# Kernel optimization log

Hardware: AMD Instinct MI355X
Metric: run time of the kernel (lower is better)

## Reference

```python
import jax, jax.numpy as jnp
import numpy as np

N = 8192
C_IN = 512
C_INTER = 128  # in_channels // unit_nums = 512 // 4


def setup_inputs() -> dict:
    key = jax.random.key(0)
    ks = jax.random.split(key, 6)
    x = jax.random.normal(ks[0], (N, C_IN), dtype=jnp.float32)
    # Linear weights init: normal(0, 0.01); biases zero. Stored as [in, out].
    Wg = 0.01 * jax.random.normal(ks[1], (C_IN, C_INTER), dtype=jnp.float32)
    Wt = 0.01 * jax.random.normal(ks[2], (C_IN, C_INTER), dtype=jnp.float32)
    Wp = 0.01 * jax.random.normal(ks[3], (C_IN, C_INTER), dtype=jnp.float32)
    bg = jnp.zeros((C_INTER,), dtype=jnp.float32)
    bt = jnp.zeros((C_INTER,), dtype=jnp.float32)
    bp = jnp.zeros((C_INTER,), dtype=jnp.float32)
    # 1x1 conv weight (1, 2*C_INTER, 1, 1) flattened: first half hits theta, second half phi
    wcat = 0.01 * jax.random.normal(ks[4], (2 * C_INTER,), dtype=jnp.float32)
    return {"x": x, "Wg": Wg, "bg": bg, "Wt": Wt, "bt": bt, "Wp": Wp, "bp": bp, "wcat": wcat}


def reference(x, Wg, bg, Wt, bt, Wp, bp, wcat):
    n = x.shape[0]
    g_x = x @ Wg + bg          # [N, C_inter]
    theta = x @ Wt + bt        # [N, C_inter]
    phi = x @ Wp + bp          # [N, C_inter]
    c = theta.shape[1]
    # 1x1 conv over cat([theta_i, phi_j]) == w1.theta_i + w2.phi_j (outer sum), then ReLU
    a = theta @ wcat[:c]       # [N]
    b = phi @ wcat[c:]         # [N]
    f = jax.nn.relu(a[:, None] + b[None, :])  # [N, N]
    z = (f / n) @ g_x          # [N, C_inter]
    return z
```

## Files before the change

kernel.cpp:

```cpp
#include <hip/hip_runtime.h>

#define C_IN   512
#define C_INT  128
#define NBUCK  8192
#define SEG    32
#define NSEG   256

typedef short short8 __attribute__((ext_vector_type(8)));
typedef float floatx4 __attribute__((ext_vector_type(4)));


__device__ __forceinline__ int bucket_of(float v, float bmin, float inv_w) {
    float fk = (v - bmin) * inv_w;
    fk = fminf(fmaxf(fk, 0.f), (float)(NBUCK - 1));
    return (int)fk;
}

__device__ __forceinline__ short bf16rnd(float v) {
    unsigned u = __float_as_uint(v);
    return (short)((u + 0x7fffu + ((u >> 16) & 1u)) >> 16);
}


__global__ __launch_bounds__(256) void prep_kernel(
        const float* __restrict__ Wt, const float* __restrict__ Wp,
        const float* __restrict__ Wg, const float* __restrict__ wcat,
        const float* __restrict__ bt, const float* __restrict__ bp,
        float* __restrict__ ut, float* __restrict__ up, float* __restrict__ scal,
        unsigned short* __restrict__ WgT) {
    int t = threadIdx.x, bk = blockIdx.x;
    if (bk < 16) {
        const float* W  = (bk < 8) ? Wt : Wp;
        const float* wv = wcat + ((bk < 8) ? 0 : C_INT);
        float* dst      = (bk < 8) ? ut : up;
        int k = (bk & 7) * 64 + (t >> 2);
        int q = t & 3;
        const float4* row = (const float4*)(W + (size_t)k * C_INT);
        const float4* cv4 = (const float4*)wv;
        float s = 0.f;
        #pragma unroll
        for (int i = 0; i < 8; ++i) {
            float4 a = row[q * 8 + i];
            float4 c = cv4[q * 8 + i];
            s += a.x * c.x + a.y * c.y + a.z * c.z + a.w * c.w;
        }
        s += __shfl_xor(s, 1);
        s += __shfl_xor(s, 2);
        if (q == 0) dst[k] = s;
    } else if (bk == 16) {
        float s1p = (t < C_INT) ? bt[t] * wcat[t] : 0.f;
        float s2p = (t < C_INT) ? bp[t] * wcat[C_INT + t] : 0.f;
        for (int off = 32; off; off >>= 1) {
            s1p += __shfl_down(s1p, off);
            s2p += __shfl_down(s2p, off);
        }
        __shared__ float red[8];
        int w = t >> 6, lane = t & 63;
        if (lane == 0) { red[w] = s1p; red[4 + w] = s2p; }
        __syncthreads();
        if (t == 0) {
            scal[0] = red[0] + red[1] + red[2] + red[3];
            scal[1] = red[4] + red[5] + red[6] + red[7];
        }
    } else {
        __shared__ float tile[64][132];
        int kb = (bk - 17) * 64;
        #pragma unroll
        for (int it = 0; it < 8; ++it) {
            int idx = it * 256 + t;
            int r = idx >> 5, c4 = idx & 31;
            *(float4*)&tile[r][c4 * 4] =
                ((const float4*)(Wg + (size_t)(kb + r) * C_INT))[c4];
        }
        __syncthreads();
        int n = t & 127, kc = (t >> 7) * 32;
        unsigned pk[16];
        #pragma unroll
        for (int i = 0; i < 16; ++i) {
            unsigned lo = (unsigned short)bf16rnd(tile[kc + 2 * i][n]);
            unsigned hi = (unsigned short)bf16rnd(tile[kc + 2 * i + 1][n]);
            pk[i] = lo | (hi << 16);
        }
        uint4* dst = (uint4*)(WgT + (size_t)n * C_IN + kb + kc);
        #pragma unroll
        for (int i2 = 0; i2 < 4; ++i2) dst[i2] = *(uint4*)&pk[i2 * 4];
    }
}


#define RSTR 66

__global__ __launch_bounds__(256) void gemm_mfma(
        const float* __restrict__ x, const unsigned short* __restrict__ WgT,
        const float* __restrict__ bg,
        const float* __restrict__ ut, const float* __restrict__ up,
        const float* __restrict__ scal,
        _Float16* __restrict__ g, float* __restrict__ a, float* __restrict__ b) {
    __shared__ float red[3][12][RSTR];
    int tid = threadIdx.x;
    int lane = tid & 63, wv = tid >> 6;
    int bx = blockIdx.x;
    int cg2 = bx >> 9;
    int i0 = (bx & 511) * 16;
    int m = lane & 15, q = lane >> 4;
    floatx4 accg[2] = {};
    floatx4 accab = {};
    const float* xrow = x + (size_t)(i0 + m) * C_IN + q * 8;
    const float* absrc = (m == 0) ? ut : up;
    #pragma unroll
    for (int ks = 0; ks < 4; ++ks) {
        int k0 = (wv * 4 + ks) * 32;
        float4 f0 = *(const float4*)(xrow + k0);
        float4 f1 = *(const float4*)(xrow + k0 + 4);
        short8 af;
        af[0] = bf16rnd(f0.x); af[1] = bf16rnd(f0.y);
        af[2] = bf16rnd(f0.z); af[3] = bf16rnd(f0.w);
        af[4] = bf16rnd(f1.x); af[5] = bf16rnd(f1.y);
        af[6] = bf16rnd(f1.z); af[7] = bf16rnd(f1.w);
        if (cg2 == 0) {
            short8 abf = {};
            if (m < 2) {
                float4 u0 = *(const float4*)(absrc + k0 + q * 8);
                float4 u1 = *(const float4*)(absrc + k0 + q * 8 + 4);
                abf[0] = bf16rnd(u0.x); abf[1] = bf16rnd(u0.y);
                abf[2] = bf16rnd(u0.z); abf[3] = bf16rnd(u0.w);
                abf[4] = bf16rnd(u1.x); abf[5] = bf16rnd(u1.y);
                abf[6] = bf16rnd(u1.z); abf[7] = bf16rnd(u1.w);
            }
            accab = __builtin_amdgcn_mfma_f32_16x16x32_bf16(af, abf, accab, 0, 0, 0);
        }
        #pragma unroll
        for (int f = 0; f < 2; ++f) {
            short8 bfr = *(const short8*)(WgT + (size_t)(cg2 * 32 + f * 16 + m) * C_IN + k0 + q * 8);
            accg[f] = __builtin_amdgcn_mfma_f32_16x16x32_bf16(af, bfr, accg[f], 0, 0, 0);
        }
    }
    if (wv) {
        #pragma unroll
        for (int f = 0; f < 2; ++f)
            #pragma unroll
            for (int r = 0; r < 4; ++r)
                red[wv - 1][f * 4 + r][lane] = accg[f][r];
        #pragma unroll
        for (int r = 0; r < 4; ++r)
            red[wv - 1][8 + r][lane] = accab[r];
    }
    __syncthreads();
    if (wv == 0) {
        #pragma unroll
        for (int w = 0; w < 3; ++w) {
            #pragma unroll
            for (int f = 0; f < 2; ++f)
                #pragma unroll
                for (int r = 0; r < 4; ++r)
                    accg[f][r] += red[w][f * 4 + r][lane];
            #pragma unroll
            for (int r = 0; r < 4; ++r)
                accab[r] += red[w][8 + r][lane];
        }
        #pragma unroll
        for (int f = 0; f < 2; ++f) {
            int col = cg2 * 32 + f * 16 + m;
            float bgv = bg[col];
            #pragma unroll
            for (int r = 0; r < 4; ++r) {
                int row = i0 + q * 4 + r;
                g[(size_t)row * C_INT + col] = (_Float16)(accg[f][r] + bgv);
            }
        }
        if (cg2 == 0 && m < 2) {
            float off = m ? scal[1] : scal[0];
            float* dst = m ? b : a;
            #pragma unroll
            for (int r = 0; r < 4; ++r) dst[i0 + q * 4 + r] = accab[r] + off;
        }
    }
}


__global__ __launch_bounds__(1024) void sort_kernel(
        const float* __restrict__ b, float* __restrict__ scal,
        unsigned* __restrict__ offs_g, unsigned short* __restrict__ perm_g,
        float* __restrict__ bsort_g) {
    __shared__ unsigned oh[NBUCK / 2];
    __shared__ unsigned cur[NBUCK / 2];
    __shared__ unsigned short ls[8192];
    __shared__ unsigned wtu[16];
    __shared__ float smn[16], smx[16], sbp[2];
    int t = threadIdx.x, lane = t & 63, wv = t >> 6;
    #pragma unroll
    for (int r = 0; r < 4; ++r) { oh[t + r * 1024] = 0u; cur[t + r * 1024] = 0u; }
    float bv[8];
    float mn = 1e30f, mx = -1e30f;
    #pragma unroll
    for (int r = 0; r < 8; ++r) {
        bv[r] = b[t + r * 1024];
        mn = fminf(mn, bv[r]); mx = fmaxf(mx, bv[r]);
    }
    for (int off = 32; off; off >>= 1) {
        mn = fminf(mn, __shfl_down(mn, off));
        mx = fmaxf(mx, __shfl_down(mx, off));
    }
    if (lane == 0) { smn[wv] = mn; smx[wv] = mx; }
    __syncthreads();
    if (t == 0) {
        float gmn = smn[0], gmx = smx[0];
        #pragma unroll
        for (int i = 1; i < 16; ++i) {
            gmn = fminf(gmn, smn[i]); gmx = fmaxf(gmx, smx[i]);
        }
        float range = gmx - gmn;
        float iw = (range > 1e-30f) ? (float)NBUCK / range : 0.f;
        sbp[0] = gmn; sbp[1] = iw;
        scal[4] = gmn; scal[5] = iw;
    }
    __syncthreads();
    float bmin = sbp[0], inv_w = sbp[1];
    int kb[8];
    #pragma unroll
    for (int r = 0; r < 8; ++r) {
        kb[r] = bucket_of(bv[r], bmin, inv_w);
        atomicAdd(&oh[kb[r] >> 1], (kb[r] & 1) ? 0x10000u : 1u);
    }
    __syncthreads();
    unsigned h[8], p = 0;
    #pragma unroll
    for (int w = 0; w < 4; ++w) {
        unsigned word = oh[t * 4 + w];
        p += word & 0xffffu;  h[w * 2]     = p;
        p += word >> 16;      h[w * 2 + 1] = p;
    }
    unsigned v = p;
    #pragma unroll
    for (int d = 1; d < 64; d <<= 1) {
        unsigned u = __shfl_up(v, d);
        if (lane >= d) v += u;
    }
    if (lane == 63) wtu[wv] = v;
    __syncthreads();
    if (t < 16) {
        unsigned w = wtu[t];
        #pragma unroll
        for (int d = 1; d < 16; d <<= 1) {
            unsigned u = __shfl_up(w, d);
            if (t >= d) w += u;
        }
        wtu[t] = w;
    }
    __syncthreads();
    unsigned base = (v - p) + (wv ? wtu[wv - 1] : 0u);
    #pragma unroll
    for (int w = 0; w < 4; ++w) {
        unsigned lo = base + h[w * 2], hi = base + h[w * 2 + 1];
        oh[t * 4 + w] = lo | (hi << 16);
        offs_g[t * 8 + w * 2 + 1] = lo;
        offs_g[t * 8 + w * 2 + 2] = hi;
    }
    if (t == 0) offs_g[0] = 0u;
    __syncthreads();
    #pragma unroll
    for (int r = 0; r < 8; ++r) {
        int j = t + r * 1024;
        int k = kb[r];
        unsigned st = 0u;
        if (k > 0) {
            unsigned word = oh[(k - 1) >> 1];
            st = ((k - 1) & 1) ? (word >> 16) : (word & 0xffffu);
        }
        unsigned old = atomicAdd(&cur[k >> 1], (k & 1) ? 0x10000u : 1u);
        unsigned pos = (k & 1) ? (old >> 16) : (old & 0xffffu);
        ls[st + pos] = (unsigned short)j;
    }
    __syncthreads();
    #pragma unroll
    for (int r = 0; r < 8; ++r) {
        int e = t + r * 1024;
        int j = ls[e];
        perm_g[e] = (unsigned short)j;
        bsort_g[e] = b[j];
    }
}


__global__ __launch_bounds__(128) void segsum_kernel(
        const _Float16* __restrict__ g, const unsigned short* __restrict__ perm,
        const float* __restrict__ bsort,
        float* __restrict__ seg1, float* __restrict__ seg2) {
    __shared__ int pj[SEG];
    __shared__ float pb[SEG];
    int s = blockIdx.x, t = threadIdx.x;
    if (t < SEG) { pj[t] = perm[s * SEG + t]; pb[t] = bsort[s * SEG + t]; }
    __syncthreads();
    float a1 = 0.f, a2 = 0.f;
    #pragma unroll
    for (int e = 0; e < SEG; ++e) {
        float gv = (float)g[(size_t)pj[e] * C_INT + t];
        a1 += gv; a2 += pb[e] * gv;
    }
    seg1[s * C_INT + t] = a1;
    seg2[s * C_INT + t] = a2;
}


__global__ __launch_bounds__(1024) void sufseg_kernel(
        const float* __restrict__ seg1, const float* __restrict__ seg2,
        float* __restrict__ Suf1, float* __restrict__ Suf2) {
    __shared__ float ps1[8][128], ps2[8][128];
    int t = threadIdx.x, u = t >> 7, c = t & 127;
    float p1 = 0.f, p2 = 0.f;
    #pragma unroll 8
    for (int j = 0; j < 32; ++j) {
        int s = u * 32 + j;
        p1 += seg1[s * C_INT + c];
        p2 += seg2[s * C_INT + c];
    }
    ps1[u][c] = p1; ps2[u][c] = p2;
    __syncthreads();
    float r1 = 0.f, r2 = 0.f;
    #pragma unroll
    for (int u2 = u + 1; u2 < 8; ++u2) { r1 += ps1[u2][c]; r2 += ps2[u2][c]; }
    for (int j = 31; j >= 0; --j) {
        int s = u * 32 + j;
        r1 += seg1[s * C_INT + c];
        r2 += seg2[s * C_INT + c];
        Suf1[s * C_INT + c] = r1;
        Suf2[s * C_INT + c] = r2;
    }
    if (t < 128) {
        Suf1[256 * C_INT + t] = 0.f; Suf2[256 * C_INT + t] = 0.f;
        Suf1[257 * C_INT + t] = 0.f; Suf2[257 * C_INT + t] = 0.f;
    }
}


__global__ __launch_bounds__(128) void out_kernel(
        const float* __restrict__ a, const float* __restrict__ scal,
        const _Float16* __restrict__ g,
        const unsigned* __restrict__ offs, const unsigned short* __restrict__ perm,
        const float* __restrict__ bsort,
        const float* __restrict__ Suf1, const float* __restrict__ Suf2,
        float* __restrict__ out, float inv_n) {
    int i = blockIdx.x, c = threadIdx.x;
    float ai = a[i], thr = -ai;
    float bmin = scal[4], inv_w = scal[5];
    int ki = bucket_of(thr, bmin, inv_w);
    unsigned e0 = offs[ki], e1 = offs[ki + 1];
    unsigned s1 = e1 >> 5;
    unsigned segend = min((s1 + 1u) * 32u, (unsigned)NBUCK);
    size_t sb = (size_t)(s1 + 1u) * C_INT + c;
    float acc = ai * Suf1[sb] + Suf2[sb];
    for (unsigned e = e1; e < segend; ++e) {
        float bj = bsort[e];
        int j = perm[e];
        acc += (ai + bj) * (float)g[(size_t)j * C_INT + c];
    }
    for (unsigned e = e0; e < e1; ++e) {
        float bj = bsort[e];
        if (bj > thr) {
            int j = perm[e];
            acc += (ai + bj) * (float)g[(size_t)j * C_INT + c];
        }
    }
    out[(size_t)i * C_INT + c] = acc * inv_n;
}


extern "C" void kernel_launch(void* const* d_in, const int* in_sizes, int n_in,
                              void* d_out, int out_size, void* d_ws, size_t ws_size,
                              hipStream_t stream) {
    const float* x    = (const float*)d_in[0];
    const float* Wg   = (const float*)d_in[1];
    const float* bg   = (const float*)d_in[2];
    const float* Wt   = (const float*)d_in[3];
    const float* bt   = (const float*)d_in[4];
    const float* Wp   = (const float*)d_in[5];
    const float* bp   = (const float*)d_in[6];
    const float* wcat = (const float*)d_in[7];
    float* out = (float*)d_out;
    int n = in_sizes[0] / C_IN;

    char* w = (char*)d_ws;
    size_t off = 0;
    auto alloc = [&](size_t bytes) -> void* {
        void* p = w + off;
        off += (bytes + 255) & ~(size_t)255;
        return p;
    };
    float*          ut    = (float*)alloc(C_IN * 4);
    float*          up    = (float*)alloc(C_IN * 4);
    float*          scal  = (float*)alloc(32);
    float*          a     = (float*)alloc((size_t)n * 4);
    float*          b     = (float*)alloc((size_t)n * 4);
    unsigned*       offs  = (unsigned*)alloc((size_t)(NBUCK + 1) * 4);
    unsigned short* perm  = (unsigned short*)alloc((size_t)n * 2);
    float*          bsort = (float*)alloc((size_t)n * 4);
    _Float16*       g     = (_Float16*)alloc((size_t)n * C_INT * 2);
    unsigned short* WgT   = (unsigned short*)alloc((size_t)C_INT * C_IN * 2);
    float*          seg1  = (float*)alloc((size_t)NSEG * C_INT * 4);
    float*          seg2  = (float*)alloc((size_t)NSEG * C_INT * 4);
    float*          Suf1  = (float*)alloc((size_t)258 * C_INT * 4);
    float*          Suf2  = (float*)alloc((size_t)258 * C_INT * 4);

    prep_kernel<<<25, 256, 0, stream>>>(Wt, Wp, Wg, wcat, bt, bp, ut, up, scal, WgT);
    gemm_mfma<<<2048, 256, 0, stream>>>(x, WgT, bg, ut, up, scal, g, a, b);
    sort_kernel<<<1, 1024, 0, stream>>>(b, scal, offs, perm, bsort);
    segsum_kernel<<<NSEG, 128, 0, stream>>>(g, perm, bsort, seg1, seg2);
    sufseg_kernel<<<1, 1024, 0, stream>>>(seg1, seg2, Suf1, Suf2);
    out_kernel<<<n, 128, 0, stream>>>(a, scal, g, offs, perm, bsort, Suf1, Suf2,
                                      out, 1.0f / (float)n);
}
```

Before: 140.4 us.

## Fuse segment-sum and suffix-scan kernels with last-block atomic completion

Merges segsum and sufseg into one kernel. The new kernel uses 32 blocks of 1024 threads, each covering 8 segments, and the last block to finish (found via an atomic counter) computes the suffix sums. This removes one kernel launch and its inter-kernel gap. The cost is fewer, larger blocks for the gather-sum phase, an extra counter reset added to prep_kernel, and reliance on threadfence ordering for correctness.

```diff
diff --git a/kernel.cpp b/kernel.cpp
--- a/kernel.cpp
+++ b/kernel.cpp
@@ -27,7 +27,7 @@
         const float* __restrict__ Wg, const float* __restrict__ wcat,
         const float* __restrict__ bt, const float* __restrict__ bp,
         float* __restrict__ ut, float* __restrict__ up, float* __restrict__ scal,
-        unsigned short* __restrict__ WgT) {
+        unsigned short* __restrict__ WgT, unsigned* __restrict__ cnt) {
     int t = threadIdx.x, bk = blockIdx.x;
     if (bk < 16) {
         const float* W  = (bk < 8) ? Wt : Wp;
@@ -62,7 +62,7 @@
             scal[0] = red[0] + red[1] + red[2] + red[3];
             scal[1] = red[4] + red[5] + red[6] + red[7];
         }
-    } else {
+    } else if (bk < 25) {
         __shared__ float tile[64][132];
         int kb = (bk - 17) * 64;
         #pragma unroll
@@ -84,6 +84,8 @@
         uint4* dst = (uint4*)(WgT + (size_t)n * C_IN + kb + kc);
         #pragma unroll
         for (int i2 = 0; i2 < 4; ++i2) dst[i2] = *(uint4*)&pk[i2 * 4];
+    } else {
+        if (t == 0) *cnt = 0u;
     }
 }
 
@@ -282,37 +284,46 @@
 }
 
 
-__global__ __launch_bounds__(128) void segsum_kernel(
+__global__ __launch_bounds__(1024) void segsum_kernel(
         const _Float16* __restrict__ g, const unsigned short* __restrict__ perm,
         const float* __restrict__ bsort,
-        float* __restrict__ seg1, float* __restrict__ seg2) {
-    __shared__ int pj[SEG];
-    __shared__ float pb[SEG];
-    int s = blockIdx.x, t = threadIdx.x;
-    if (t < SEG) { pj[t] = perm[s * SEG + t]; pb[t] = bsort[s * SEG + t]; }
-    __syncthreads();
+        float* __restrict__ seg1, float* __restrict__ seg2,
+        float* __restrict__ Suf1, float* __restrict__ Suf2,
+        unsigned* __restrict__ cnt) {
+    __shared__ int pj[8][SEG];
+    __shared__ float pb[8][SEG];
+    __shared__ float ps1[8][128], ps2[8][128];
+    __shared__ unsigned lastFlag;
+    int blk = blockIdx.x, t = threadIdx.x;
+    int u = t >> 7, c = t & 127;
+    if (t < 256) {
+        pj[t >> 5][t & 31] = perm[blk * 256 + t];
+        pb[t >> 5][t & 31] = bsort[blk * 256 + t];
+    }
+    __syncthreads();
+    int s = blk * 8 + u;
     float a1 = 0.f, a2 = 0.f;
     #pragma unroll
     for (int e = 0; e < SEG; ++e) {
-        float gv = (float)g[(size_t)pj[e] * C_INT + t];
-        a1 += gv; a2 += pb[e] * gv;
-    }
-    seg1[s * C_INT + t] = a1;
-    seg2[s * C_INT + t] = a2;
-}
-
-
-__global__ __launch_bounds__(1024) void sufseg_kernel(
-        const float* __restrict__ seg1, const float* __restrict__ seg2,
-        float* __restrict__ Suf1, float* __restrict__ Suf2) {
-    __shared__ float ps1[8][128], ps2[8][128];
-    int t = threadIdx.x, u = t >> 7, c = t & 127;
+        float gv = (float)g[(size_t)pj[u][e] * C_INT + c];
+        a1 += gv; a2 += pb[u][e] * gv;
+    }
+    seg1[s * C_INT + c] = a1;
+    seg2[s * C_INT + c] = a2;
+    __threadfence();
+    __syncthreads();
+    if (t == 0)
+        lastFlag = (__hip_atomic_fetch_add(cnt, 1u, __ATOMIC_ACQ_REL,
+                                           __HIP_MEMORY_SCOPE_AGENT) == 31u);
+    __syncthreads();
+    if (!lastFlag) return;
+    __threadfence();
     float p1 = 0.f, p2 = 0.f;
     #pragma unroll 8
     for (int j = 0; j < 32; ++j) {
-        int s = u * 32 + j;
-        p1 += seg1[s * C_INT + c];
-        p2 += seg2[s * C_INT + c];
+        int s2 = u * 32 + j;
+        p1 += seg1[s2 * C_INT + c];
+        p2 += seg2[s2 * C_INT + c];
     }
     ps1[u][c] = p1; ps2[u][c] = p2;
     __syncthreads();
@@ -320,11 +331,11 @@
     #pragma unroll
     for (int u2 = u + 1; u2 < 8; ++u2) { r1 += ps1[u2][c]; r2 += ps2[u2][c]; }
     for (int j = 31; j >= 0; --j) {
-        int s = u * 32 + j;
-        r1 += seg1[s * C_INT + c];
-        r2 += seg2[s * C_INT + c];
-        Suf1[s * C_INT + c] = r1;
-        Suf2[s * C_INT + c] = r2;
+        int s2 = u * 32 + j;
+        r1 += seg1[s2 * C_INT + c];
+        r2 += seg2[s2 * C_INT + c];
+        Suf1[s2 * C_INT + c] = r1;
+        Suf2[s2 * C_INT + c] = r2;
     }
     if (t < 128) {
         Suf1[256 * C_INT + t] = 0.f; Suf2[256 * C_INT + t] = 0.f;
@@ -400,12 +411,14 @@
     float*          seg2  = (float*)alloc((size_t)NSEG * C_INT * 4);
     float*          Suf1  = (float*)alloc((size_t)258 * C_INT * 4);
     float*          Suf2  = (float*)alloc((size_t)258 * C_INT * 4);
-
-    prep_kernel<<<25, 256, 0, stream>>>(Wt, Wp, Wg, wcat, bt, bp, ut, up, scal, WgT);
+    unsigned*       cnt   = (unsigned*)alloc(256);
+
+    prep_kernel<<<26, 256, 0, stream>>>(Wt, Wp, Wg, wcat, bt, bp, ut, up, scal,
+                                        WgT, cnt);
     gemm_mfma<<<2048, 256, 0, stream>>>(x, WgT, bg, ut, up, scal, g, a, b);
     sort_kernel<<<1, 1024, 0, stream>>>(b, scal, offs, perm, bsort);
-    segsum_kernel<<<NSEG, 128, 0, stream>>>(g, perm, bsort, seg1, seg2);
-    sufseg_kernel<<<1, 1024, 0, stream>>>(seg1, seg2, Suf1, Suf2);
+    segsum_kernel<<<32, 1024, 0, stream>>>(g, perm, bsort, seg1, seg2,
+                                           Suf1, Suf2, cnt);
     out_kernel<<<n, 128, 0, stream>>>(a, scal, g, offs, perm, bsort, Suf1, Suf2,
                                       out, 1.0f / (float)n);
 }
```

Result: slower. 156.4 us (+11.4%).

## Fuse sort into the GEMM launch and compute a/b projections in prep

Applied to the files above, without the earlier changes.

The projections a and b are now computed in fp32 inside the prep kernel. Each of its 128 blocks recomputes the folded theta/phi weight vectors, then takes dot products with its rows of x. The single-block bucket sort now runs as block 0 of a combined launch whose other blocks do the g GEMM, so the sort can overlap the GEMM instead of running alone as a serial kernel. In exchange, x is read twice, the folded weights are recomputed redundantly per block, and the GEMM now uses 1024-thread blocks that share one LDS union with the sort.

```diff
diff --git a/kernel.cpp b/kernel.cpp
--- a/kernel.cpp
+++ b/kernel.cpp
@@ -26,45 +26,57 @@
         const float* __restrict__ Wt, const float* __restrict__ Wp,
         const float* __restrict__ Wg, const float* __restrict__ wcat,
         const float* __restrict__ bt, const float* __restrict__ bp,
-        float* __restrict__ ut, float* __restrict__ up, float* __restrict__ scal,
+        const float* __restrict__ x,
+        float* __restrict__ a, float* __restrict__ b,
         unsigned short* __restrict__ WgT) {
     int t = threadIdx.x, bk = blockIdx.x;
-    if (bk < 16) {
-        const float* W  = (bk < 8) ? Wt : Wp;
-        const float* wv = wcat + ((bk < 8) ? 0 : C_INT);
-        float* dst      = (bk < 8) ? ut : up;
-        int k = (bk & 7) * 64 + (t >> 2);
-        int q = t & 3;
-        const float4* row = (const float4*)(W + (size_t)k * C_INT);
-        const float4* cv4 = (const float4*)wv;
-        float s = 0.f;
-        #pragma unroll
-        for (int i = 0; i < 8; ++i) {
-            float4 a = row[q * 8 + i];
-            float4 c = cv4[q * 8 + i];
-            s += a.x * c.x + a.y * c.y + a.z * c.z + a.w * c.w;
-        }
-        s += __shfl_xor(s, 1);
-        s += __shfl_xor(s, 2);
-        if (q == 0) dst[k] = s;
-    } else if (bk == 16) {
-        float s1p = (t < C_INT) ? bt[t] * wcat[t] : 0.f;
-        float s2p = (t < C_INT) ? bp[t] * wcat[C_INT + t] : 0.f;
-        for (int off = 32; off; off >>= 1) {
-            s1p += __shfl_down(s1p, off);
-            s2p += __shfl_down(s2p, off);
-        }
-        __shared__ float red[8];
-        int w = t >> 6, lane = t & 63;
-        if (lane == 0) { red[w] = s1p; red[4 + w] = s2p; }
-        __syncthreads();
-        if (t == 0) {
-            scal[0] = red[0] + red[1] + red[2] + red[3];
-            scal[1] = red[4] + red[5] + red[6] + red[7];
-        }
+    if (bk < 128) {
+        __shared__ float utl[512], upl[512];
+        __shared__ float sred[2];
+        #pragma unroll
+        for (int h = 0; h < 2; ++h) {
+            int k = t + h * 256;
+            const float4* wr = (const float4*)(Wt + (size_t)k * C_INT);
+            const float4* pr = (const float4*)(Wp + (size_t)k * C_INT);
+            const float4* c1 = (const float4*)wcat;
+            const float4* c2 = (const float4*)(wcat + C_INT);
+            float s1 = 0.f, s2 = 0.f;
+            #pragma unroll
+            for (int j = 0; j < 32; ++j) {
+                float4 w4 = wr[j], q4 = pr[j], a4 = c1[j], b4 = c2[j];
+                s1 += w4.x * a4.x + w4.y * a4.y + w4.z * a4.z + w4.w * a4.w;
+                s2 += q4.x * b4.x + q4.y * b4.y + q4.z * b4.z + q4.w * b4.w;
+            }
+            utl[k] = s1; upl[k] = s2;
+        }
+        {
+            float v = 0.f;
+            if (t < 64)        v = bt[t] * wcat[t] + bt[t + 64] * wcat[t + 64];
+            else if (t < 128) { int c = t - 64;
+                               v = bp[c] * wcat[C_INT + c] + bp[c + 64] * wcat[C_INT + c + 64]; }
+            for (int off = 32; off; off >>= 1) v += __shfl_down(v, off);
+            if (t < 128 && (t & 63) == 0) sred[t >> 6] = v;
+        }
+        __syncthreads();
+        float s0 = sred[0], s1c = sred[1];
+        int r = t >> 2, kq = t & 3;
+        int i = bk * 64 + r;
+        const float4* xr = (const float4*)(x + (size_t)i * C_IN + kq * 128);
+        const float4* u4 = (const float4*)(utl + kq * 128);
+        const float4* p4 = (const float4*)(upl + kq * 128);
+        float sa = 0.f, sb = 0.f;
+        #pragma unroll
+        for (int j = 0; j < 32; ++j) {
+            float4 xv = xr[j], uv = u4[j], pv = p4[j];
+            sa += xv.x * uv.x + xv.y * uv.y + xv.z * uv.z + xv.w * uv.w;
+            sb += xv.x * pv.x + xv.y * pv.y + xv.z * pv.z + xv.w * pv.w;
+        }
+        sa += __shfl_xor(sa, 1); sa += __shfl_xor(sa, 2);
+        sb += __shfl_xor(sb, 1); sb += __shfl_xor(sb, 2);
+        if (kq == 0) { a[i] = sa + s0; b[i] = sb + s1c; }
     } else {
         __shared__ float tile[64][132];
-        int kb = (bk - 17) * 64;
+        int kb = (bk - 128) * 64;
         #pragma unroll
         for (int it = 0; it < 8; ++it) {
             int idx = it * 256 + t;
@@ -90,194 +102,175 @@
 
 #define RSTR 66
 
-__global__ __launch_bounds__(256) void gemm_mfma(
+struct SortLDS {
+    unsigned oh[NBUCK / 2];
+    unsigned cur[NBUCK / 2];
+    unsigned short ls[8192];
+    unsigned wtu[16];
+    float smn[16], smx[16], sbp[2];
+};
+
+__global__ __launch_bounds__(1024) void gst_kernel(
         const float* __restrict__ x, const unsigned short* __restrict__ WgT,
-        const float* __restrict__ bg,
-        const float* __restrict__ ut, const float* __restrict__ up,
-        const float* __restrict__ scal,
-        _Float16* __restrict__ g, float* __restrict__ a, float* __restrict__ b) {
-    __shared__ float red[3][12][RSTR];
-    int tid = threadIdx.x;
-    int lane = tid & 63, wv = tid >> 6;
-    int bx = blockIdx.x;
-    int cg2 = bx >> 9;
-    int i0 = (bx & 511) * 16;
-    int m = lane & 15, q = lane >> 4;
-    floatx4 accg[2] = {};
-    floatx4 accab = {};
-    const float* xrow = x + (size_t)(i0 + m) * C_IN + q * 8;
-    const float* absrc = (m == 0) ? ut : up;
-    #pragma unroll
-    for (int ks = 0; ks < 4; ++ks) {
-        int k0 = (wv * 4 + ks) * 32;
-        float4 f0 = *(const float4*)(xrow + k0);
-        float4 f1 = *(const float4*)(xrow + k0 + 4);
-        short8 af;
-        af[0] = bf16rnd(f0.x); af[1] = bf16rnd(f0.y);
-        af[2] = bf16rnd(f0.z); af[3] = bf16rnd(f0.w);
-        af[4] = bf16rnd(f1.x); af[5] = bf16rnd(f1.y);
-        af[6] = bf16rnd(f1.z); af[7] = bf16rnd(f1.w);
-        if (cg2 == 0) {
-            short8 abf = {};
-            if (m < 2) {
-                float4 u0 = *(const float4*)(absrc + k0 + q * 8);
-                float4 u1 = *(const float4*)(absrc + k0 + q * 8 + 4);
-                abf[0] = bf16rnd(u0.x); abf[1] = bf16rnd(u0.y);
-                abf[2] = bf16rnd(u0.z); abf[3] = bf16rnd(u0.w);
-                abf[4] = bf16rnd(u1.x); abf[5] = bf16rnd(u1.y);
-                abf[6] = bf16rnd(u1.z); abf[7] = bf16rnd(u1.w);
-            }
-            accab = __builtin_amdgcn_mfma_f32_16x16x32_bf16(af, abf, accab, 0, 0, 0);
-        }
-        #pragma unroll
-        for (int f = 0; f < 2; ++f) {
-            short8 bfr = *(const short8*)(WgT + (size_t)(cg2 * 32 + f * 16 + m) * C_IN + k0 + q * 8);
-            accg[f] = __builtin_amdgcn_mfma_f32_16x16x32_bf16(af, bfr, accg[f], 0, 0, 0);
-        }
-    }
-    if (wv) {
-        #pragma unroll
-        for (int f = 0; f < 2; ++f)
-            #pragma unroll
-            for (int r = 0; r < 4; ++r)
-                red[wv - 1][f * 4 + r][lane] = accg[f][r];
-        #pragma unroll
-        for (int r = 0; r < 4; ++r)
-            red[wv - 1][8 + r][lane] = accab[r];
-    }
-    __syncthreads();
-    if (wv == 0) {
-        #pragma unroll
-        for (int w = 0; w < 3; ++w) {
+        const float* __restrict__ bg, const float* __restrict__ b,
+        float* __restrict__ scal, unsigned* __restrict__ offs_g,
+        unsigned short* __restrict__ perm_g, float* __restrict__ bsort_g,
+        _Float16* __restrict__ g) {
+    __shared__ union {
+        SortLDS s;
+        float red[4][3][8][RSTR];
+    } u;
+    int blk = blockIdx.x, t = threadIdx.x;
+
+    if (blk == 0) {
+        unsigned* oh = u.s.oh;
+        unsigned* cur = u.s.cur;
+        unsigned short* ls = u.s.ls;
+        unsigned* wtu = u.s.wtu;
+        float* smn = u.s.smn; float* smx = u.s.smx; float* sbp = u.s.sbp;
+        int lane = t & 63, wv = t >> 6;
+        #pragma unroll
+        for (int r = 0; r < 4; ++r) { oh[t + r * 1024] = 0u; cur[t + r * 1024] = 0u; }
+        float bv[8];
+        float mn = 1e30f, mx = -1e30f;
+        #pragma unroll
+        for (int r = 0; r < 8; ++r) {
+            bv[r] = b[t + r * 1024];
+            mn = fminf(mn, bv[r]); mx = fmaxf(mx, bv[r]);
+        }
+        for (int off = 32; off; off >>= 1) {
+            mn = fminf(mn, __shfl_down(mn, off));
+            mx = fmaxf(mx, __shfl_down(mx, off));
+        }
+        if (lane == 0) { smn[wv] = mn; smx[wv] = mx; }
+        __syncthreads();
+        if (t == 0) {
+            float gmn = smn[0], gmx = smx[0];
+            #pragma unroll
+            for (int i = 1; i < 16; ++i) {
+                gmn = fminf(gmn, smn[i]); gmx = fmaxf(gmx, smx[i]);
+            }
+            float range = gmx - gmn;
+            float iw = (range > 1e-30f) ? (float)NBUCK / range : 0.f;
+            sbp[0] = gmn; sbp[1] = iw;
+            scal[4] = gmn; scal[5] = iw;
+        }
+        __syncthreads();
+        float bmin = sbp[0], inv_w = sbp[1];
+        int kb[8];
+        #pragma unroll
+        for (int r = 0; r < 8; ++r) {
+            kb[r] = bucket_of(bv[r], bmin, inv_w);
+            atomicAdd(&oh[kb[r] >> 1], (kb[r] & 1) ? 0x10000u : 1u);
+        }
+        __syncthreads();
+        unsigned h[8], p = 0;
+        #pragma unroll
+        for (int w = 0; w < 4; ++w) {
+            unsigned word = oh[t * 4 + w];
+            p += word & 0xffffu;  h[w * 2]     = p;
+            p += word >> 16;      h[w * 2 + 1] = p;
+        }
+        unsigned v = p;
+        #pragma unroll
+        for (int d = 1; d < 64; d <<= 1) {
+            unsigned uu = __shfl_up(v, d);
+            if (lane >= d) v += uu;
+        }
+        if (lane == 63) wtu[wv] = v;
+        __syncthreads();
+        if (t < 16) {
+            unsigned w = wtu[t];
+            #pragma unroll
+            for (int d = 1; d < 16; d <<= 1) {
+                unsigned uu = __shfl_up(w, d);
+                if (t >= d) w += uu;
+            }
+            wtu[t] = w;
+        }
+        __syncthreads();
+        unsigned base = (v - p) + (wv ? wtu[wv - 1] : 0u);
+        #pragma unroll
+        for (int w = 0; w < 4; ++w) {
+            unsigned lo = base + h[w * 2], hi = base + h[w * 2 + 1];
+            oh[t * 4 + w] = lo | (hi << 16);
+            offs_g[t * 8 + w * 2 + 1] = lo;
+            offs_g[t * 8 + w * 2 + 2] = hi;
+        }
+        if (t == 0) offs_g[0] = 0u;
+        __syncthreads();
+        #pragma unroll
+        for (int r = 0; r < 8; ++r) {
+            int j = t + r * 1024;
+            int k = kb[r];
+            unsigned st = 0u;
+            if (k > 0) {
+                unsigned word = oh[(k - 1) >> 1];
+                st = ((k - 1) & 1) ? (word >> 16) : (word & 0xffffu);
+            }
+            unsigned old = atomicAdd(&cur[k >> 1], (k & 1) ? 0x10000u : 1u);
+            unsigned pos = (k & 1) ? (old >> 16) : (old & 0xffffu);
+            ls[st + pos] = (unsigned short)j;
+        }
+        __syncthreads();
+        #pragma unroll
+        for (int r = 0; r < 8; ++r) {
+            int e = t + r * 1024;
+            int j = ls[e];
+            perm_g[e] = (unsigned short)j;
+            bsort_g[e] = b[j];
+        }
+    } else {
+        int grp = t >> 8, tl = t & 255;
+        int lane = tl & 63, wv = tl >> 6;
+        int cg2 = grp;
+        int i0 = (blk - 1) * 16;
+        int m = lane & 15, q = lane >> 4;
+        floatx4 accg[2] = {};
+        const float* xrow = x + (size_t)(i0 + m) * C_IN + q * 8;
+        #pragma unroll
+        for (int ks = 0; ks < 4; ++ks) {
+            int k0 = (wv * 4 + ks) * 32;
+            float4 f0 = *(const float4*)(xrow + k0);
+            float4 f1 = *(const float4*)(xrow + k0 + 4);
+            short8 af;
+            af[0] = bf16rnd(f0.x); af[1] = bf16rnd(f0.y);
+            af[2] = bf16rnd(f0.z); af[3] = bf16rnd(f0.w);
+            af[4] = bf16rnd(f1.x); af[5] = bf16rnd(f1.y);
+            af[6] = bf16rnd(f1.z); af[7] = bf16rnd(f1.w);
+            #pragma unroll
+            for (int f = 0; f < 2; ++f) {
+                short8 bfr = *(const short8*)(WgT + (size_t)(cg2 * 32 + f * 16 + m) * C_IN + k0 + q * 8);
+                accg[f] = __builtin_amdgcn_mfma_f32_16x16x32_bf16(af, bfr, accg[f], 0, 0, 0);
+            }
+        }
+        if (wv) {
             #pragma unroll
             for (int f = 0; f < 2; ++f)
                 #pragma unroll
                 for (int r = 0; r < 4; ++r)
-                    accg[f][r] += red[w][f * 4 + r][lane];
-            #pragma unroll
-            for (int r = 0; r < 4; ++r)
-                accab[r] += red[w][8 + r][lane];
-        }
-        #pragma unroll
-        for (int f = 0; f < 2; ++f) {
-            int col = cg2 * 32 + f * 16 + m;
-            float bgv = bg[col];
-            #pragma unroll
-            for (int r = 0; r < 4; ++r) {
-                int row = i0 + q * 4 + r;
-                g[(size_t)row * C_INT + col] = (_Float16)(accg[f][r] + bgv);
-            }
-        }
-        if (cg2 == 0 && m < 2) {
-            float off = m ? scal[1] : scal[0];
-            float* dst = m ? b : a;
-            #pragma unroll
-            for (int r = 0; r < 4; ++r) dst[i0 + q * 4 + r] = accab[r] + off;
-        }
-    }
-}
-
-
-__global__ __launch_bounds__(1024) void sort_kernel(
-        const float* __restrict__ b, float* __restrict__ scal,
-        unsigned* __restrict__ offs_g, unsigned short* __restrict__ perm_g,
-        float* __restrict__ bsort_g) {
-    __shared__ unsigned oh[NBUCK / 2];
-    __shared__ unsigned cur[NBUCK / 2];
-    __shared__ unsigned short ls[8192];
-    __shared__ unsigned wtu[16];
-    __shared__ float smn[16], smx[16], sbp[2];
-    int t = threadIdx.x, lane = t & 63, wv = t >> 6;
-    #pragma unroll
-    for (int r = 0; r < 4; ++r) { oh[t + r * 1024] = 0u; cur[t + r * 1024] = 0u; }
-    float bv[8];
-    float mn = 1e30f, mx = -1e30f;
-    #pragma unroll
-    for (int r = 0; r < 8; ++r) {
-        bv[r] = b[t + r * 1024];
-        mn = fminf(mn, bv[r]); mx = fmaxf(mx, bv[r]);
-    }
-    for (int off = 32; off; off >>= 1) {
-        mn = fminf(mn, __shfl_down(mn, off));
-        mx = fmaxf(mx, __shfl_down(mx, off));
-    }
-    if (lane == 0) { smn[wv] = mn; smx[wv] = mx; }
-    __syncthreads();
-    if (t == 0) {
-        float gmn = smn[0], gmx = smx[0];
-        #pragma unroll
-        for (int i = 1; i < 16; ++i) {
-            gmn = fminf(gmn, smn[i]); gmx = fmaxf(gmx, smx[i]);
-        }
-        float range = gmx - gmn;
-        float iw = (range > 1e-30f) ? (float)NBUCK / range : 0.f;
-        sbp[0] = gmn; sbp[1] = iw;
-        scal[4] = gmn; scal[5] = iw;
-    }
-    __syncthreads();
-    float bmin = sbp[0], inv_w = sbp[1];
-    int kb[8];
-    #pragma unroll
-    for (int r = 0; r < 8; ++r) {
-        kb[r] = bucket_of(bv[r], bmin, inv_w);
-        atomicAdd(&oh[kb[r] >> 1], (kb[r] & 1) ? 0x10000u : 1u);
-    }
-    __syncthreads();
-    unsigned h[8], p = 0;
-    #pragma unroll
-    for (int w = 0; w < 4; ++w) {
-        unsigned word = oh[t * 4 + w];
-        p += word & 0xffffu;  h[w * 2]     = p;
-        p += word >> 16;      h[w * 2 + 1] = p;
-    }
-    unsigned v = p;
-    #pragma unroll
-    for (int d = 1; d < 64; d <<= 1) {
-        unsigned u = __shfl_up(v, d);
-        if (lane >= d) v += u;
-    }
-    if (lane == 63) wtu[wv] = v;
-    __syncthreads();
-    if (t < 16) {
-        unsigned w = wtu[t];
-        #pragma unroll
-        for (int d = 1; d < 16; d <<= 1) {
-            unsigned u = __shfl_up(w, d);
-            if (t >= d) w += u;
-        }
-        wtu[t] = w;
-    }
-    __syncthreads();
-    unsigned base = (v - p) + (wv ? wtu[wv - 1] : 0u);
-    #pragma unroll
-    for (int w = 0; w < 4; ++w) {
-        unsigned lo = base + h[w * 2], hi = base + h[w * 2 + 1];
-        oh[t * 4 + w] = lo | (hi << 16);
-        offs_g[t * 8 + w * 2 + 1] = lo;
-        offs_g[t * 8 + w * 2 + 2] = hi;
-    }
-    if (t == 0) offs_g[0] = 0u;
-    __syncthreads();
-    #pragma unroll
-    for (int r = 0; r < 8; ++r) {
-        int j = t + r * 1024;
-        int k = kb[r];
-        unsigned st = 0u;
-        if (k > 0) {
-            unsigned word = oh[(k - 1) >> 1];
-            st = ((k - 1) & 1) ? (word >> 16) : (word & 0xffffu);
-        }
-        unsigned old = atomicAdd(&cur[k >> 1], (k & 1) ? 0x10000u : 1u);
-        unsigned pos = (k & 1) ? (old >> 16) : (old & 0xffffu);
-        ls[st + pos] = (unsigned short)j;
-    }
-    __syncthreads();
-    #pragma unroll
-    for (int r = 0; r < 8; ++r) {
-        int e = t + r * 1024;
-        int j = ls[e];
-        perm_g[e] = (unsigned short)j;
-        bsort_g[e] = b[j];
+                    u.red[grp][wv - 1][f * 4 + r][lane] = accg[f][r];
+        }
+        __syncthreads();
+        if (wv == 0) {
+            #pragma unroll
+            for (int w = 0; w < 3; ++w)
+                #pragma unroll
+                for (int f = 0; f < 2; ++f)
+                    #pragma unroll
+                    for (int r = 0; r < 4; ++r)
+                        accg[f][r] += u.red[grp][w][f * 4 + r][lane];
+            #pragma unroll
+            for (int f = 0; f < 2; ++f) {
+                int col = cg2 * 32 + f * 16 + m;
+                float bgv = bg[col];
+                #pragma unroll
+                for (int r = 0; r < 4; ++r) {
+                    int row = i0 + q * 4 + r;
+                    g[(size_t)row * C_INT + col] = (_Float16)(accg[f][r] + bgv);
+                }
+            }
+        }
     }
 }
 
@@ -386,8 +379,6 @@
         off += (bytes + 255) & ~(size_t)255;
         return p;
     };
-    float*          ut    = (float*)alloc(C_IN * 4);
-    float*          up    = (float*)alloc(C_IN * 4);
     float*          scal  = (float*)alloc(32);
     float*          a     = (float*)alloc((size_t)n * 4);
     float*          b     = (float*)alloc((size_t)n * 4);
@@ -401,9 +392,8 @@
     float*          Suf1  = (float*)alloc((size_t)258 * C_INT * 4);
     float*          Suf2  = (float*)alloc((size_t)258 * C_INT * 4);
 
-    prep_kernel<<<25, 256, 0, stream>>>(Wt, Wp, Wg, wcat, bt, bp, ut, up, scal, WgT);
-    gemm_mfma<<<2048, 256, 0, stream>>>(x, WgT, bg, ut, up, scal, g, a, b);
-    sort_kernel<<<1, 1024, 0, stream>>>(b, scal, offs, perm, bsort);
+    prep_kernel<<<136, 256, 0, stream>>>(Wt, Wp, Wg, wcat, bt, bp, x, a, b, WgT);
+    gst_kernel<<<513, 1024, 0, stream>>>(x, WgT, bg, b, scal, offs, perm, bsort, g);
     segsum_kernel<<<NSEG, 128, 0, stream>>>(g, perm, bsort, seg1, seg2);
     sufseg_kernel<<<1, 1024, 0, stream>>>(seg1, seg2, Suf1, Suf2);
     out_kernel<<<n, 128, 0, stream>>>(a, scal, g, offs, perm, bsort, Suf1, Suf2,
```

Measured after the change: 162.2 us. 1.16x slower.
